# Optimization experiments

Hardware: AMD Instinct MI355X
Metric: run time of the kernel (lower is better)

Reference implementation:

```python
import jax, jax.numpy as jnp
import numpy as np

B, S, D, H = 2, 2048, 1024, 16
DK = D // H


def setup_inputs() -> dict:
    key = jax.random.key(0)
    ks = jax.random.split(key, 11)
    s = 1.0 / np.sqrt(D)
    return {
        "q": jax.random.normal(ks[0], (B, S, D), jnp.float32),
        "k": jax.random.normal(ks[1], (B, S, D), jnp.float32),
        "v": jax.random.normal(ks[2], (B, S, D), jnp.float32),
        "mask": jnp.ones((B, 1, S, S), jnp.int32),
        "Wq": jax.random.normal(ks[3], (D, D), jnp.float32) * s,
        "bq": jnp.zeros((D,), jnp.float32),
        "Wk": jax.random.normal(ks[4], (D, D), jnp.float32) * s,
        "bk": jnp.zeros((D,), jnp.float32),
        "Wv": jax.random.normal(ks[5], (D, D), jnp.float32) * s,
        "bv": jnp.zeros((D,), jnp.float32),
        "Wo": jax.random.normal(ks[6], (D, D), jnp.float32) * s,
        "bo": jnp.zeros((D,), jnp.float32),
    }


def reference(q, k, v, mask, Wq, bq, Wk, bk, Wv, bv, Wo, bo):
    # Note: original torch code calls non-in-place masked_fill and discards the
    # result, so the mask has no mathematical effect; we preserve that.
    qh = (q @ Wq + bq).reshape(B, S, H, DK).transpose(0, 2, 1, 3)  # [B,H,S,DK]
    kh = (k @ Wk + bk).reshape(B, S, H, DK).transpose(0, 2, 1, 3)
    vh = (v @ Wv + bv).reshape(B, S, H, DK).transpose(0, 2, 1, 3)
    scores = jnp.einsum("bhqd,bhkd->bhqk", qh, kh) / jnp.sqrt(jnp.float32(DK))
    attn = jax.nn.softmax(scores, axis=-1)
    out = jnp.einsum("bhqk,bhkd->bhqd", attn, vh)  # [B,H,S,DK]
    out = out.transpose(0, 2, 1, 3).reshape(B, S, D)
    return out @ Wo + bo
```

## Files before the change

### kernel.cpp

```cpp
#include <hip/hip_runtime.h>

#define S_LEN    2048
#define D_MODEL  1024
#define N_HEADS  16
#define HEAD_DIM 64
#define BATCH    2

typedef __bf16 bf16x8 __attribute__((ext_vector_type(8)));
typedef float  floatx4 __attribute__((ext_vector_type(4)));

__device__ __forceinline__ unsigned short f2bf(float f) {
    union { float f; unsigned int u; } v;
    v.f = f;
    unsigned int u = v.u;
    u += 0x7fffu + ((u >> 16) & 1u);
    return (unsigned short)(u >> 16);
}

__device__ __forceinline__ unsigned int pk_bf16(float a, float b) {
    union { float f; unsigned int u; } ua, ub;
    ua.f = a; ub.f = b;
    unsigned int x = ua.u + (0x7fffu + ((ua.u >> 16) & 1u));
    unsigned int y = ub.u + (0x7fffu + ((ub.u >> 16) & 1u));
    return (x >> 16) | (y & 0xffff0000u);
}

__device__ __forceinline__ void gload_lds16(const unsigned short* g, unsigned short* l) {
    __builtin_amdgcn_global_load_lds(
        (const __attribute__((address_space(1))) void*)(const void*)g,
        (__attribute__((address_space(3))) void*)(void*)l,
        16, 0, 0);
}

struct Conv3Args { const float* src[3]; unsigned short* dst[3]; };

__global__ void conv3_kernel(Conv3Args args, int n4) {
    int i = blockIdx.x * blockDim.x + threadIdx.x;
    const float* src = args.src[blockIdx.y];
    unsigned short* dst = args.dst[blockIdx.y];
    if (i < n4) {
        float4 f = reinterpret_cast<const float4*>(src)[i];
        ushort4 o;
        o.x = f2bf(f.x); o.y = f2bf(f.y); o.z = f2bf(f.z); o.w = f2bf(f.w);
        reinterpret_cast<ushort4*>(dst)[i] = o;
    }
}

struct Tr4Args { const float* W[4]; unsigned short* Wt[4]; };

__global__ void transpose4_kernel(Tr4Args args) {
    __shared__ unsigned short tile[64][65];
    const float* W = args.W[blockIdx.z];
    unsigned short* Wt = args.Wt[blockIdx.z];
    int n0 = blockIdx.x * 64, k0 = blockIdx.y * 64;
    for (int rep = 0; rep < 16; ++rep) {
        int e = rep * 256 + threadIdx.x;
        int kk = e >> 6, nn = e & 63;
        tile[kk][nn] = f2bf(W[(size_t)(k0 + kk) * D_MODEL + n0 + nn]);
    }
    __syncthreads();
    for (int rep = 0; rep < 16; ++rep) {
        int e = rep * 256 + threadIdx.x;
        int nn = e >> 6, kk = e & 63;
        Wt[(size_t)(n0 + nn) * D_MODEL + k0 + kk] = tile[kk][nn];
    }
}

template <int TM, int TN, int MODE>
__device__ __forceinline__
void gemm_body(const unsigned short* __restrict__ A,
               const unsigned short* __restrict__ Bt,
               const float* __restrict__ bias,
               void* __restrict__ out,
               int m0, int n0,
               unsigned short* As, unsigned short* Bs) {
    constexpr int MT = TM / 32;
    constexpr int NT = TN / 32;
    const int tid  = threadIdx.x;
    const int wid  = tid >> 6;
    const int lane = tid & 63;

    floatx4 acc[MT][NT];
#pragma unroll
    for (int i = 0; i < MT; ++i)
#pragma unroll
        for (int j = 0; j < NT; ++j) acc[i][j] = (floatx4)0.0f;

    const int srow = lane >> 2;
    const int gch  = (lane & 3) ^ ((srow >> 1) & 3);
    const int wr = (wid >> 1) * (TM / 2);
    const int wc = (wid & 1) * (TN / 2);
    const int fr = lane & 15;
    const int fq = lane >> 4;
    const int swz = (fq ^ ((fr >> 1) & 3)) * 8;

    for (int k0 = 0; k0 < D_MODEL; k0 += 32) {
        if (k0) __syncthreads();
#pragma unroll
        for (int ci = 0; ci < (TM + TN) / 64; ++ci) {
            const int c = wid + ci * 4;
            if (c < TM / 16) {
                const int row = c * 16 + srow;
                gload_lds16(A + (size_t)(m0 + row) * D_MODEL + k0 + gch * 8, As + c * 512);
            } else {
                const int cb = c - TM / 16;
                const int row = cb * 16 + srow;
                gload_lds16(Bt + (size_t)(n0 + row) * D_MODEL + k0 + gch * 8, Bs + cb * 512);
            }
        }
        __syncthreads();

        bf16x8 af[MT], bfv[NT];
#pragma unroll
        for (int t = 0; t < MT; ++t)
            af[t] = *reinterpret_cast<const bf16x8*>(As + (wr + t * 16 + fr) * 32 + swz);
#pragma unroll
        for (int t = 0; t < NT; ++t)
            bfv[t] = *reinterpret_cast<const bf16x8*>(Bs + (wc + t * 16 + fr) * 32 + swz);
#pragma unroll
        for (int mt = 0; mt < MT; ++mt)
#pragma unroll
            for (int nt = 0; nt < NT; ++nt)
                acc[mt][nt] = __builtin_amdgcn_mfma_f32_16x16x32_bf16(af[mt], bfv[nt], acc[mt][nt], 0, 0, 0);
    }

#pragma unroll
    for (int nt = 0; nt < NT; ++nt) {
        const int n = n0 + wc + nt * 16 + fr;
        const float bval = bias[n];
#pragma unroll
        for (int mt = 0; mt < MT; ++mt) {
#pragma unroll
            for (int r = 0; r < 4; ++r) {
                const int m = m0 + wr + mt * 16 + fq * 4 + r;
                const float val = acc[mt][nt][r] + bval;
                if (MODE == 2) {
                    reinterpret_cast<float*>(out)[(size_t)m * D_MODEL + n] = val;
                } else {
                    const int b = m >> 11, s = m & (S_LEN - 1);
                    const int h = n >> 6, dk = n & 63;
                    const unsigned short o16 = f2bf(val);
                    if (MODE == 0)
                        reinterpret_cast<unsigned short*>(out)[(((size_t)(b * N_HEADS + h)) * S_LEN + s) * HEAD_DIM + dk] = o16;
                    else
                        reinterpret_cast<unsigned short*>(out)[(((size_t)(b * N_HEADS + h)) * HEAD_DIM + dk) * S_LEN + s] = o16;
                }
            }
        }
    }
}

struct QKVArgs {
    const unsigned short* A[3];
    const unsigned short* Bt[3];
    const float* bias[3];
    unsigned short* out[3];
};

__global__ __launch_bounds__(256)
void qkv_gemm_kernel(QKVArgs args) {
    __shared__ __align__(16) unsigned short As[128 * 32];
    __shared__ __align__(16) unsigned short Bs[128 * 32];
    const int z = blockIdx.z;
    const int m0 = blockIdx.y * 128;
    const int n0 = blockIdx.x * 128;
    if (z == 2)
        gemm_body<128, 128, 1>(args.A[2], args.Bt[2], args.bias[2], args.out[2], m0, n0, As, Bs);
    else
        gemm_body<128, 128, 0>(args.A[z], args.Bt[z], args.bias[z], args.out[z], m0, n0, As, Bs);
}

__global__ __launch_bounds__(256)
void oproj_gemm_kernel(const unsigned short* __restrict__ A,
                       const unsigned short* __restrict__ Bt,
                       const float* __restrict__ bias,
                       float* __restrict__ out) {
    __shared__ __align__(16) unsigned short As[64 * 32];
    __shared__ __align__(16) unsigned short Bs[128 * 32];
    gemm_body<64, 128, 2>(A, Bt, bias, out, blockIdx.y * 64, blockIdx.x * 128, As, Bs);
}

__global__ __launch_bounds__(256)
void attn_kernel(const unsigned short* __restrict__ qh,
                 const unsigned short* __restrict__ kh,
                 const unsigned short* __restrict__ vt,
                 unsigned short* __restrict__ outp) {
    __shared__ __align__(16) unsigned short Qs[64 * 64];
    __shared__ __align__(16) unsigned short Ks[64 * 64];
    __shared__ __align__(16) unsigned short Vs[64 * 64];
    __shared__ __align__(16) unsigned short Ps[4][16 * 72];

    const int tid  = threadIdx.x;
    const int wid  = tid >> 6;
    const int lane = tid & 63;
    const int b = blockIdx.z, h = blockIdx.y;
    const int q0 = blockIdx.x * 64;

    const unsigned short* qbase = qh + (size_t)(b * N_HEADS + h) * S_LEN * HEAD_DIM;
    const unsigned short* kbase = kh + (size_t)(b * N_HEADS + h) * S_LEN * HEAD_DIM;
    const unsigned short* vbase = vt + (size_t)(b * N_HEADS + h) * HEAD_DIM * S_LEN;

    const int srow = lane >> 3;
    const int gch  = (lane & 7) ^ srow;
    const int fr = lane & 15;
    const int fq = lane >> 4;
    const int sw7 = fr & 7;

#pragma unroll
    for (int i = 0; i < 2; ++i) {
        const int c = wid + i * 4;
        const int row = c * 8 + srow;
        gload_lds16(qbase + (size_t)(q0 + row) * HEAD_DIM + gch * 8, Qs + c * 512);
    }
    __syncthreads();

    bf16x8 qf[2];
#pragma unroll
    for (int kk = 0; kk < 2; ++kk)
        qf[kk] = *reinterpret_cast<const bf16x8*>(
            Qs + (wid * 16 + fr) * 64 + (((kk * 4 + fq) ^ sw7) * 8));

    floatx4 o_acc[4];
#pragma unroll
    for (int i = 0; i < 4; ++i) o_acc[i] = (floatx4)0.0f;
    float l_sum = 0.0f;

    for (int kv0 = 0; kv0 < S_LEN; kv0 += 64) {
        if (kv0) __syncthreads();
#pragma unroll
        for (int i = 0; i < 2; ++i) {
            const int c = wid + i * 4;
            const int row = c * 8 + srow;
            gload_lds16(kbase + (size_t)(kv0 + row) * HEAD_DIM + gch * 8, Ks + c * 512);
            gload_lds16(vbase + (size_t)row * S_LEN + kv0 + gch * 8,       Vs + c * 512);
        }
        __syncthreads();

        floatx4 st[4];
#pragma unroll
        for (int i = 0; i < 4; ++i) st[i] = (floatx4)0.0f;
#pragma unroll
        for (int nt = 0; nt < 4; ++nt) {
#pragma unroll
            for (int kk = 0; kk < 2; ++kk) {
                bf16x8 kf = *reinterpret_cast<const bf16x8*>(
                    Ks + (nt * 16 + fr) * 64 + (((kk * 4 + fq) ^ sw7) * 8));
                st[nt] = __builtin_amdgcn_mfma_f32_16x16x32_bf16(kf, qf[kk], st[nt], 0, 0, 0);
            }
        }

#pragma unroll
        for (int nt = 0; nt < 4; ++nt) {
            const float c = 0.18033688f;
            float p0 = __builtin_amdgcn_exp2f(st[nt][0] * c);
            float p1 = __builtin_amdgcn_exp2f(st[nt][1] * c);
            float p2 = __builtin_amdgcn_exp2f(st[nt][2] * c);
            float p3 = __builtin_amdgcn_exp2f(st[nt][3] * c);
            l_sum += (p0 + p1) + (p2 + p3);
            uint2 w;
            w.x = pk_bf16(p0, p1);
            w.y = pk_bf16(p2, p3);
            *reinterpret_cast<uint2*>(Ps[wid] + fr * 72 + nt * 16 + fq * 4) = w;
        }
        __asm__ volatile("s_waitcnt lgkmcnt(0)" ::: "memory");

#pragma unroll
        for (int kk = 0; kk < 2; ++kk) {
            bf16x8 pf = *reinterpret_cast<const bf16x8*>(Ps[wid] + fr * 72 + kk * 32 + fq * 8);
#pragma unroll
            for (int dt = 0; dt < 4; ++dt) {
                bf16x8 vf = *reinterpret_cast<const bf16x8*>(
                    Vs + (dt * 16 + fr) * 64 + (((kk * 4 + fq) ^ sw7) * 8));
                o_acc[dt] = __builtin_amdgcn_mfma_f32_16x16x32_bf16(pf, vf, o_acc[dt], 0, 0, 0);
            }
        }
    }

    l_sum += __shfl_xor(l_sum, 16);
    l_sum += __shfl_xor(l_sum, 32);

    float linv[4];
#pragma unroll
    for (int r = 0; r < 4; ++r)
        linv[r] = __builtin_amdgcn_rcpf(__shfl(l_sum, fq * 4 + r));
#pragma unroll
    for (int dt = 0; dt < 4; ++dt) {
#pragma unroll
        for (int r = 0; r < 4; ++r) {
            const int s  = q0 + wid * 16 + fq * 4 + r;
            const int dk = dt * 16 + fr;
            const float val = o_acc[dt][r] * linv[r];
            outp[((size_t)(b * S_LEN + s)) * D_MODEL + h * HEAD_DIM + dk] = f2bf(val);
        }
    }
}

extern "C" void kernel_launch(void* const* d_in, const int* in_sizes, int n_in,
                              void* d_out, int out_size, void* d_ws, size_t ws_size,
                              hipStream_t stream) {
    (void)in_sizes; (void)n_in; (void)out_size; (void)ws_size;
    const float* q  = (const float*)d_in[0];
    const float* k  = (const float*)d_in[1];
    const float* v  = (const float*)d_in[2];
    const float* Wq = (const float*)d_in[4];
    const float* bq = (const float*)d_in[5];
    const float* Wk = (const float*)d_in[6];
    const float* bk = (const float*)d_in[7];
    const float* Wv = (const float*)d_in[8];
    const float* bv = (const float*)d_in[9];
    const float* Wo = (const float*)d_in[10];
    const float* bo = (const float*)d_in[11];
    float* out = (float*)d_out;

    char* ws = (char*)d_ws;
    const size_t SZ_ACT = (size_t)BATCH * S_LEN * D_MODEL * 2;
    const size_t SZ_W   = (size_t)D_MODEL * D_MODEL * 2;
    unsigned short* qb   = (unsigned short*)(ws);
    unsigned short* kb   = (unsigned short*)(ws + SZ_ACT);
    unsigned short* vb   = (unsigned short*)(ws + 2 * SZ_ACT);
    unsigned short* Wqt  = (unsigned short*)(ws + 3 * SZ_ACT);
    unsigned short* Wkt  = (unsigned short*)(ws + 3 * SZ_ACT + SZ_W);
    unsigned short* Wvt  = (unsigned short*)(ws + 3 * SZ_ACT + 2 * SZ_W);
    unsigned short* Wot  = (unsigned short*)(ws + 3 * SZ_ACT + 3 * SZ_W);
    unsigned short* qhb  = (unsigned short*)(ws + 3 * SZ_ACT + 4 * SZ_W);
    unsigned short* khb  = (unsigned short*)(ws + 4 * SZ_ACT + 4 * SZ_W);
    unsigned short* vtb  = (unsigned short*)(ws + 5 * SZ_ACT + 4 * SZ_W);
    unsigned short* attn = qb;

    const int n4 = BATCH * S_LEN * D_MODEL / 4;

    Conv3Args cargs;
    cargs.src[0] = q;  cargs.src[1] = k;  cargs.src[2] = v;
    cargs.dst[0] = qb; cargs.dst[1] = kb; cargs.dst[2] = vb;
    conv3_kernel<<<dim3(n4 / 256, 3), 256, 0, stream>>>(cargs, n4);

    Tr4Args targs;
    targs.W[0] = Wq;  targs.W[1] = Wk;  targs.W[2] = Wv;  targs.W[3] = Wo;
    targs.Wt[0] = Wqt; targs.Wt[1] = Wkt; targs.Wt[2] = Wvt; targs.Wt[3] = Wot;
    transpose4_kernel<<<dim3(16, 16, 4), 256, 0, stream>>>(targs);

    QKVArgs gargs;
    gargs.A[0] = qb;  gargs.A[1] = kb;  gargs.A[2] = vb;
    gargs.Bt[0] = Wqt; gargs.Bt[1] = Wkt; gargs.Bt[2] = Wvt;
    gargs.bias[0] = bq; gargs.bias[1] = bk; gargs.bias[2] = bv;
    gargs.out[0] = qhb; gargs.out[1] = khb; gargs.out[2] = vtb;
    qkv_gemm_kernel<<<dim3(8, 32, 3), 256, 0, stream>>>(gargs);

    attn_kernel<<<dim3(S_LEN / 64, N_HEADS, BATCH), 256, 0, stream>>>(qhb, khb, vtb, attn);

    oproj_gemm_kernel<<<dim3(8, 64), 256, 0, stream>>>(attn, Wot, bo, out);
}
```

Before: 269.5 us.

## Double attention query tile per block and fold softmax scale into Q projection

Each attention block now handles 128 queries, two 16-row tiles per wave, so every K/V tile loaded into LDS is reused across twice as many queries and half as many blocks launch. The softmax scale (1/sqrt(dk)·log2e) is applied in the Q-projection epilogue, removing the per-element multiply before exp2 in the attention loop. The bf16 pair packing now uses a single byte-permute instruction. The cost is more registers and LDS per block, which may lower occupancy, and fewer blocks in flight (512 instead of 1024).

```diff
diff --git a/kernel.cpp b/kernel.cpp
--- a/kernel.cpp
+++ b/kernel.cpp
@@ -17,12 +17,12 @@
     return (unsigned short)(u >> 16);
 }
 
-__device__ __forceinline__ unsigned int pk_bf16(float a, float b) {
+__device__ __forceinline__ unsigned int pk_rne(float a, float b) {
     union { float f; unsigned int u; } ua, ub;
     ua.f = a; ub.f = b;
-    unsigned int x = ua.u + (0x7fffu + ((ua.u >> 16) & 1u));
-    unsigned int y = ub.u + (0x7fffu + ((ub.u >> 16) & 1u));
-    return (x >> 16) | (y & 0xffff0000u);
+    unsigned int x = ua.u + 0x7fffu + ((ua.u >> 16) & 1u);
+    unsigned int y = ub.u + 0x7fffu + ((ub.u >> 16) & 1u);
+    return __builtin_amdgcn_perm(y, x, 0x07060302);
 }
 
 __device__ __forceinline__ void gload_lds16(const unsigned short* g, unsigned short* l) {
@@ -72,7 +72,7 @@
                const unsigned short* __restrict__ Bt,
                const float* __restrict__ bias,
                void* __restrict__ out,
-               int m0, int n0,
+               int m0, int n0, float scale,
                unsigned short* As, unsigned short* Bs) {
     constexpr int MT = TM / 32;
     constexpr int NT = TN / 32;
@@ -133,7 +133,7 @@
 #pragma unroll
             for (int r = 0; r < 4; ++r) {
                 const int m = m0 + wr + mt * 16 + fq * 4 + r;
-                const float val = acc[mt][nt][r] + bval;
+                const float val = (acc[mt][nt][r] + bval) * scale;
                 if (MODE == 2) {
                     reinterpret_cast<float*>(out)[(size_t)m * D_MODEL + n] = val;
                 } else {
@@ -164,10 +164,12 @@
     const int z = blockIdx.z;
     const int m0 = blockIdx.y * 128;
     const int n0 = blockIdx.x * 128;
-    if (z == 2)
-        gemm_body<128, 128, 1>(args.A[2], args.Bt[2], args.bias[2], args.out[2], m0, n0, As, Bs);
+    if (z == 0)
+        gemm_body<128, 128, 0>(args.A[0], args.Bt[0], args.bias[0], args.out[0], m0, n0, 0.18033688011112f, As, Bs);
+    else if (z == 1)
+        gemm_body<128, 128, 0>(args.A[1], args.Bt[1], args.bias[1], args.out[1], m0, n0, 1.0f, As, Bs);
     else
-        gemm_body<128, 128, 0>(args.A[z], args.Bt[z], args.bias[z], args.out[z], m0, n0, As, Bs);
+        gemm_body<128, 128, 1>(args.A[2], args.Bt[2], args.bias[2], args.out[2], m0, n0, 1.0f, As, Bs);
 }
 
 __global__ __launch_bounds__(256)
@@ -177,28 +179,28 @@
                        float* __restrict__ out) {
     __shared__ __align__(16) unsigned short As[64 * 32];
     __shared__ __align__(16) unsigned short Bs[128 * 32];
-    gemm_body<64, 128, 2>(A, Bt, bias, out, blockIdx.y * 64, blockIdx.x * 128, As, Bs);
+    gemm_body<64, 128, 2>(A, Bt, bias, out, blockIdx.y * 64, blockIdx.x * 128, 1.0f, As, Bs);
 }
 
 __global__ __launch_bounds__(256)
-void attn_kernel(const unsigned short* __restrict__ qh,
-                 const unsigned short* __restrict__ kh,
-                 const unsigned short* __restrict__ vt,
+void attn_kernel(const unsigned short* __restrict__ qhp,
+                 const unsigned short* __restrict__ khp,
+                 const unsigned short* __restrict__ vtp,
                  unsigned short* __restrict__ outp) {
-    __shared__ __align__(16) unsigned short Qs[64 * 64];
+    __shared__ __align__(16) unsigned short Qs[128 * 64];
     __shared__ __align__(16) unsigned short Ks[64 * 64];
     __shared__ __align__(16) unsigned short Vs[64 * 64];
-    __shared__ __align__(16) unsigned short Ps[4][16 * 72];
+    __shared__ __align__(16) unsigned short Ps[4][32 * 72];
 
     const int tid  = threadIdx.x;
     const int wid  = tid >> 6;
     const int lane = tid & 63;
     const int b = blockIdx.z, h = blockIdx.y;
-    const int q0 = blockIdx.x * 64;
-
-    const unsigned short* qbase = qh + (size_t)(b * N_HEADS + h) * S_LEN * HEAD_DIM;
-    const unsigned short* kbase = kh + (size_t)(b * N_HEADS + h) * S_LEN * HEAD_DIM;
-    const unsigned short* vbase = vt + (size_t)(b * N_HEADS + h) * HEAD_DIM * S_LEN;
+    const int q0 = blockIdx.x * 128;
+
+    const unsigned short* qbase = qhp + (size_t)(b * N_HEADS + h) * S_LEN * HEAD_DIM;
+    const unsigned short* kbase = khp + (size_t)(b * N_HEADS + h) * S_LEN * HEAD_DIM;
+    const unsigned short* vbase = vtp + (size_t)(b * N_HEADS + h) * HEAD_DIM * S_LEN;
 
     const int srow = lane >> 3;
     const int gch  = (lane & 7) ^ srow;
@@ -207,23 +209,27 @@
     const int sw7 = fr & 7;
 
 #pragma unroll
-    for (int i = 0; i < 2; ++i) {
+    for (int i = 0; i < 4; ++i) {
         const int c = wid + i * 4;
         const int row = c * 8 + srow;
         gload_lds16(qbase + (size_t)(q0 + row) * HEAD_DIM + gch * 8, Qs + c * 512);
     }
     __syncthreads();
 
-    bf16x8 qf[2];
-#pragma unroll
-    for (int kk = 0; kk < 2; ++kk)
-        qf[kk] = *reinterpret_cast<const bf16x8*>(
-            Qs + (wid * 16 + fr) * 64 + (((kk * 4 + fq) ^ sw7) * 8));
-
-    floatx4 o_acc[4];
-#pragma unroll
-    for (int i = 0; i < 4; ++i) o_acc[i] = (floatx4)0.0f;
-    float l_sum = 0.0f;
+    bf16x8 qf[2][2];
+#pragma unroll
+    for (int qh2 = 0; qh2 < 2; ++qh2)
+#pragma unroll
+        for (int kk = 0; kk < 2; ++kk)
+            qf[qh2][kk] = *reinterpret_cast<const bf16x8*>(
+                Qs + (wid * 32 + qh2 * 16 + fr) * 64 + (((kk * 4 + fq) ^ sw7) * 8));
+
+    floatx4 o_acc[2][4];
+#pragma unroll
+    for (int i = 0; i < 2; ++i)
+#pragma unroll
+        for (int j = 0; j < 4; ++j) o_acc[i][j] = (floatx4)0.0f;
+    float l_sum[2] = {0.0f, 0.0f};
 
     for (int kv0 = 0; kv0 < S_LEN; kv0 += 64) {
         if (kv0) __syncthreads();
@@ -236,61 +242,71 @@
         }
         __syncthreads();
 
-        floatx4 st[4];
-#pragma unroll
-        for (int i = 0; i < 4; ++i) st[i] = (floatx4)0.0f;
+        floatx4 st[2][4];
+#pragma unroll
+        for (int i = 0; i < 2; ++i)
+#pragma unroll
+            for (int j = 0; j < 4; ++j) st[i][j] = (floatx4)0.0f;
 #pragma unroll
         for (int nt = 0; nt < 4; ++nt) {
 #pragma unroll
             for (int kk = 0; kk < 2; ++kk) {
                 bf16x8 kf = *reinterpret_cast<const bf16x8*>(
                     Ks + (nt * 16 + fr) * 64 + (((kk * 4 + fq) ^ sw7) * 8));
-                st[nt] = __builtin_amdgcn_mfma_f32_16x16x32_bf16(kf, qf[kk], st[nt], 0, 0, 0);
-            }
-        }
-
-#pragma unroll
-        for (int nt = 0; nt < 4; ++nt) {
-            const float c = 0.18033688f;
-            float p0 = __builtin_amdgcn_exp2f(st[nt][0] * c);
-            float p1 = __builtin_amdgcn_exp2f(st[nt][1] * c);
-            float p2 = __builtin_amdgcn_exp2f(st[nt][2] * c);
-            float p3 = __builtin_amdgcn_exp2f(st[nt][3] * c);
-            l_sum += (p0 + p1) + (p2 + p3);
-            uint2 w;
-            w.x = pk_bf16(p0, p1);
-            w.y = pk_bf16(p2, p3);
-            *reinterpret_cast<uint2*>(Ps[wid] + fr * 72 + nt * 16 + fq * 4) = w;
+                st[0][nt] = __builtin_amdgcn_mfma_f32_16x16x32_bf16(kf, qf[0][kk], st[0][nt], 0, 0, 0);
+                st[1][nt] = __builtin_amdgcn_mfma_f32_16x16x32_bf16(kf, qf[1][kk], st[1][nt], 0, 0, 0);
+            }
+        }
+
+#pragma unroll
+        for (int qh2 = 0; qh2 < 2; ++qh2) {
+#pragma unroll
+            for (int nt = 0; nt < 4; ++nt) {
+                float p0 = __builtin_amdgcn_exp2f(st[qh2][nt][0]);
+                float p1 = __builtin_amdgcn_exp2f(st[qh2][nt][1]);
+                float p2 = __builtin_amdgcn_exp2f(st[qh2][nt][2]);
+                float p3 = __builtin_amdgcn_exp2f(st[qh2][nt][3]);
+                l_sum[qh2] += (p0 + p1) + (p2 + p3);
+                uint2 w;
+                w.x = pk_rne(p0, p1);
+                w.y = pk_rne(p2, p3);
+                *reinterpret_cast<uint2*>(Ps[wid] + (qh2 * 16 + fr) * 72 + nt * 16 + fq * 4) = w;
+            }
         }
         __asm__ volatile("s_waitcnt lgkmcnt(0)" ::: "memory");
 
 #pragma unroll
         for (int kk = 0; kk < 2; ++kk) {
-            bf16x8 pf = *reinterpret_cast<const bf16x8*>(Ps[wid] + fr * 72 + kk * 32 + fq * 8);
+            bf16x8 pf0 = *reinterpret_cast<const bf16x8*>(Ps[wid] + (fr)      * 72 + kk * 32 + fq * 8);
+            bf16x8 pf1 = *reinterpret_cast<const bf16x8*>(Ps[wid] + (16 + fr) * 72 + kk * 32 + fq * 8);
 #pragma unroll
             for (int dt = 0; dt < 4; ++dt) {
                 bf16x8 vf = *reinterpret_cast<const bf16x8*>(
                     Vs + (dt * 16 + fr) * 64 + (((kk * 4 + fq) ^ sw7) * 8));
-                o_acc[dt] = __builtin_amdgcn_mfma_f32_16x16x32_bf16(pf, vf, o_acc[dt], 0, 0, 0);
-            }
-        }
-    }
-
-    l_sum += __shfl_xor(l_sum, 16);
-    l_sum += __shfl_xor(l_sum, 32);
-
-    float linv[4];
-#pragma unroll
-    for (int r = 0; r < 4; ++r)
-        linv[r] = __builtin_amdgcn_rcpf(__shfl(l_sum, fq * 4 + r));
-#pragma unroll
-    for (int dt = 0; dt < 4; ++dt) {
-#pragma unroll
-        for (int r = 0; r < 4; ++r) {
-            const int s  = q0 + wid * 16 + fq * 4 + r;
-            const int dk = dt * 16 + fr;
-            const float val = o_acc[dt][r] * linv[r];
-            outp[((size_t)(b * S_LEN + s)) * D_MODEL + h * HEAD_DIM + dk] = f2bf(val);
+                o_acc[0][dt] = __builtin_amdgcn_mfma_f32_16x16x32_bf16(pf0, vf, o_acc[0][dt], 0, 0, 0);
+                o_acc[1][dt] = __builtin_amdgcn_mfma_f32_16x16x32_bf16(pf1, vf, o_acc[1][dt], 0, 0, 0);
+            }
+        }
+    }
+
+#pragma unroll
+    for (int qh2 = 0; qh2 < 2; ++qh2) {
+        float l = l_sum[qh2];
+        l += __shfl_xor(l, 16);
+        l += __shfl_xor(l, 32);
+        float linv[4];
+#pragma unroll
+        for (int r = 0; r < 4; ++r)
+            linv[r] = __builtin_amdgcn_rcpf(__shfl(l, fq * 4 + r));
+#pragma unroll
+        for (int dt = 0; dt < 4; ++dt) {
+#pragma unroll
+            for (int r = 0; r < 4; ++r) {
+                const int s  = q0 + wid * 32 + qh2 * 16 + fq * 4 + r;
+                const int dk = dt * 16 + fr;
+                const float val = o_acc[qh2][dt][r] * linv[r];
+                outp[((size_t)(b * S_LEN + s)) * D_MODEL + h * HEAD_DIM + dk] = f2bf(val);
+            }
         }
     }
 }
@@ -346,7 +362,7 @@
     gargs.out[0] = qhb; gargs.out[1] = khb; gargs.out[2] = vtb;
     qkv_gemm_kernel<<<dim3(8, 32, 3), 256, 0, stream>>>(gargs);
 
-    attn_kernel<<<dim3(S_LEN / 64, N_HEADS, BATCH), 256, 0, stream>>>(qhb, khb, vtb, attn);
+    attn_kernel<<<dim3(S_LEN / 128, N_HEADS, BATCH), 256, 0, stream>>>(qhb, khb, vtb, attn);
 
     oproj_gemm_kernel<<<dim3(8, 64), 256, 0, stream>>>(attn, Wot, bo, out);
 }
```

After: 261.2 us. 1.03x faster.
